# Optimization experiments

Hardware: AMD Instinct MI355X
Metric: run time of the kernel (lower is better)

Reference implementation:

```python
import jax, jax.numpy as jnp
import numpy as np

# SSD Detect post-processing constants (match init_kwargs)
NUM_CLASSES = 21
TOP_K = 200
CONF_THRESH = 0.95
NMS_THRESH = 0.45
M_CAND = 600      # candidate cap; chosen so all boxes passing CONF_THRESH fit (~437 expected)
NEG = -1e30


def setup_inputs() -> dict:
    key = jax.random.key(0)
    k1, k2, k3 = jax.random.split(key, 3)
    B, P, C = 8, 8732, NUM_CLASSES
    loc_data = jax.random.normal(k1, (B, P, 4), dtype=jnp.float32)
    conf_data = jax.random.uniform(k2, (B, P, C), dtype=jnp.float32)
    prior_data = jax.random.uniform(k3, (1, P, 4), dtype=jnp.float32)
    return {"loc_data": loc_data, "conf_data": conf_data, "prior_data": prior_data}


def _nms_lane(boxes_all, scores):
    """One (batch, class) lane. boxes_all: [P,4], scores: [P]. Returns [TOP_K, 5]."""
    pass_mask = scores > CONF_THRESH                       # [P]
    masked = jnp.where(pass_mask, scores, jnp.float32(NEG))
    vals, idx = jax.lax.top_k(masked, M_CAND)              # score-desc candidates (prior idx)
    valid = vals > jnp.float32(NEG / 2)                    # passed threshold
    cb = boxes_all[idx]                                    # [M,4] (x1,y1,x2,y2)
    x1, y1, x2, y2 = cb[:, 0], cb[:, 1], cb[:, 2], cb[:, 3]
    area = (x2 - x1) * (y2 - y1)                           # torchvision-style, no clamp
    xx1 = jnp.maximum(x1[:, None], x1[None, :])
    yy1 = jnp.maximum(y1[:, None], y1[None, :])
    xx2 = jnp.minimum(x2[:, None], x2[None, :])
    yy2 = jnp.minimum(y2[:, None], y2[None, :])
    inter = jnp.clip(xx2 - xx1, 0.0) * jnp.clip(yy2 - yy1, 0.0)
    iou = inter / (area[:, None] + area[None, :] - inter)  # [M,M]
    ar = jnp.arange(M_CAND)

    def body(i, supp):
        keep_i = valid[i] & jnp.logical_not(supp[i])
        return supp | (keep_i & (iou[i] > NMS_THRESH) & (ar > i))

    supp = jax.lax.fori_loop(0, M_CAND, body, jnp.zeros((M_CAND,), bool))
    keep = valid & jnp.logical_not(supp)
    order = jnp.argsort(jnp.logical_not(keep))             # stable: kept first, score order
    n = jnp.minimum(keep.sum(), TOP_K)                     # number of kept boxes (<= TOP_K)
    sel_prior = idx[order[:TOP_K]]                         # prior ids of kept (score order)
    slot_valid = jnp.arange(TOP_K) < n
    fp = jnp.argmax(pass_mask)                             # first prior passing threshold
    prior_ids = jnp.where(slot_valid, sel_prior, fp)       # pad with boxes[0] like torch
    out_scores = jnp.where(slot_valid, scores[prior_ids], 0.0)
    out = jnp.concatenate([out_scores[:, None], boxes_all[prior_ids]], axis=1)  # [K,5]
    return jnp.where(pass_mask.any(), out, jnp.zeros_like(out))


def _forward(loc_data, conf_data, prior_data):
    # prior_data is accepted per the torch signature but unused by the forward math.
    per_batch = jax.vmap(
        lambda boxes, conf_b: jax.vmap(lambda s: _nms_lane(boxes, s))(conf_b[:, 1:].T)
    )
    out_fg = per_batch(loc_data, conf_data)                # [B, C-1, K, 5]
    bg = jnp.zeros_like(out_fg[:, :1])                     # background class row stays 0
    return jnp.concatenate([bg, out_fg], axis=1)           # [B, C, K, 5]


def reference(loc_data, conf_data, prior_data):
    return _forward(loc_data, conf_data, prior_data)
```

## Files before the change

### kernel.cpp

```cpp
#include <hip/hip_runtime.h>
#include <float.h>
#include <math.h>


#define P_PRIORS  8732
#define C_CLASSES 21
#define B_BATCH   8
#define TOPK      200
#define MCAND     600
#define CONF_T    0.95f
#define NMS_T     0.45f
#define NB        64
#define MINB      0x3F733334u

__device__ __forceinline__ uint64_t pack_key(float sc, int p) {
    return ((uint64_t)__float_as_uint(sc) << 32) | (uint32_t)(~(uint32_t)p);
}
__device__ __forceinline__ int bucket_of(uint64_t key) {
    unsigned d = (unsigned)(key >> 32) - MINB;
    int b = (int)(d >> 14);
    return b < (NB - 1) ? b : (NB - 1);
}

#define IOU_ROW(BI, AI, MW, DIAG) do {                                   \
    float xx1 = fmaxf((BI).x, bj.x);                                     \
    float yy1 = fmaxf((BI).y, bj.y);                                     \
    float xx2 = fminf((BI).z, bj.z);                                     \
    float yy2 = fminf((BI).w, bj.w);                                     \
    float ww  = fmaxf(xx2 - xx1, 0.0f);                                  \
    float hh  = fmaxf(yy2 - yy1, 0.0f);                                  \
    float inter = ww * hh;                                               \
    float den   = ((AI) + aj) - inter;              \
    float iou   = inter / den;               \
    uint64_t m = __ballot(iou > NMS_T);                                  \
    if (k == c) m &= (DIAG);                                             \
    (MW) = (lid == k) ? m : (MW);                                        \
} while (0)

__device__ __forceinline__ void iou_chunk(
    int c, int wid, int lid, int M, int kmax,
    const float4* s_jb, const float* s_area, uint64_t* s_bm)
{
    const int i0 = (c << 6) + wid;
    const float4 b0 = s_jb[i0],      b1 = s_jb[i0 + 16],
                 b2 = s_jb[i0 + 32], b3 = s_jb[i0 + 48];
    const float  a0 = s_area[i0],      a1 = s_area[i0 + 16],
                 a2 = s_area[i0 + 32], a3 = s_area[i0 + 48];
    const uint64_t d0 = ~0ull << (wid + 1);
    const uint64_t d1 = ~0ull << (wid + 17);
    const uint64_t d2 = ~0ull << (wid + 33);
    const uint64_t d3 = (wid == 15) ? 0ull : (~0ull << (wid + 49));
    uint64_t w0 = 0, w1 = 0, w2 = 0, w3 = 0;
    for (int k = c; k < kmax; ++k) {
        const float4 bj = s_jb[(k << 6) + lid];
        const float  aj = s_area[(k << 6) + lid];
        IOU_ROW(b0, a0, w0, d0);
        IOU_ROW(b1, a1, w1, d1);
        IOU_ROW(b2, a2, w2, d2);
        IOU_ROW(b3, a3, w3, d3);
    }
    if (lid >= c && lid < kmax) {
        if (i0      < M) s_bm[(size_t)(i0     ) * 10 + lid] = w0;
        if (i0 + 16 < M) s_bm[(size_t)(i0 + 16) * 10 + lid] = w1;
        if (i0 + 32 < M) s_bm[(size_t)(i0 + 32) * 10 + lid] = w2;
        if (i0 + 48 < M) s_bm[(size_t)(i0 + 48) * 10 + lid] = w3;
    }
}

__global__ __launch_bounds__(1024) void detect_one(
    const float* __restrict__ loc, const float* __restrict__ conf,
    float* __restrict__ out)
{
    const int b   = blockIdx.x & 7;
    const int cls = blockIdx.x >> 3;
    const int tid = threadIdx.x;
    float* o = out + ((size_t)(b * C_CLASSES + cls)) * TOPK * 5;

    if (cls == 0) {
        for (int k = tid; k < TOPK * 5; k += 1024) o[k] = 0.0f;
        return;
    }

    const float*  confb = conf + (size_t)b * P_PRIORS * C_CLASSES + cls;
    const float4* loc4  = (const float4*)(loc + (size_t)b * P_PRIORS * 4);

    __shared__ uint64_t s_bm[MCAND * 10];
    __shared__ float4   s_jb[640];
    __shared__ float    s_area[640];
    __shared__ float    s_ssc[MCAND];
    __shared__ int      s_bcnt[NB], s_bcur[NB], s_boff[NB];
    __shared__ int      s_cnt, s_fp;
    __shared__ uint64_t s_suppw[10], s_keepw[10];
    __shared__ int      s_prefix[10], s_n, s_mstop, s_done;

    uint64_t* s_k   = s_bm;
    uint64_t* s_g   = s_bm + 1024;
    uint64_t* s_srt = s_bm + 2048;

    if (tid < NB)                    s_bcnt[tid] = 0;
    else if (tid < 2 * NB)           s_bcur[tid - NB] = 0;
    else if (tid == 2 * NB)        { s_cnt = 0; s_fp = 0x7FFFFFFF; }
    __syncthreads();

    {
        const int lid = tid & 63;
        for (int p = tid; p < P_PRIORS; p += 1024) {
            float sc = confb[(size_t)p * C_CLASSES];
            bool pass = sc > CONF_T;
            uint64_t mask = __ballot(pass);
            if (mask != 0) {
                int leader = (int)__ffsll((unsigned long long)mask) - 1;
                int base = 0;
                if (lid == leader) {
                    base = atomicAdd(&s_cnt, __popcll(mask));
                    atomicMin(&s_fp, p);
                }
                base = __shfl(base, leader, 64);
                if (pass) {
                    int pos = base + __popcll(mask & ((1ull << lid) - 1ull));
                    if (pos < 1024) s_k[pos] = pack_key(sc, p);
                }
            }
        }
    }
    __syncthreads();
    int cnt = s_cnt; if (cnt > 1024) cnt = 1024;
    if (cnt == 0) {
        for (int k = tid; k < TOPK * 5; k += 1024) o[k] = 0.0f;
        return;
    }

    for (int t = tid; t < cnt; t += 1024)
        atomicAdd(&s_bcnt[bucket_of(s_k[t])], 1);
    __syncthreads();

    if (tid < 64) {
        int c = s_bcnt[63 - tid];
        int incl = c;
        #pragma unroll
        for (int d = 1; d < 64; d <<= 1) {
            int u = __shfl_up(incl, d, 64);
            if (tid >= d) incl += u;
        }
        s_boff[63 - tid] = incl - c;
    }
    __syncthreads();

    for (int t = tid; t < cnt; t += 1024) {
        uint64_t kt = s_k[t];
        int bb = bucket_of(kt);
        s_g[s_boff[bb] + atomicAdd(&s_bcur[bb], 1)] = kt;
    }
    __syncthreads();

    const int M = cnt < MCAND ? cnt : MCAND;
    {
        const int wid = tid >> 6, lid = tid & 63;
        for (int bb = wid; bb < NB; bb += 16) {
            int st = s_boff[bb], n = s_bcnt[bb];
            for (int e = lid; e < n; e += 64) {
                uint64_t kq = s_g[st + e];
                int r = st;
                for (int q = 0; q < n; ++q)
                    r += (s_g[st + q] > kq) ? 1 : 0;
                if (r < MCAND) s_srt[r] = kq;
            }
        }
    }
    __syncthreads();

    for (int i = tid; i < M; i += 1024) {
        uint64_t key = s_srt[i];
        int p = (int)(~(uint32_t)key);
        s_ssc[i]  = __uint_as_float((uint32_t)(key >> 32));
        float4 bx = loc4[p];
        s_jb[i]   = bx;
        s_area[i] = (bx.z - bx.x) * (bx.w - bx.y);
    }
    for (int i = M + tid; i < 640; i += 1024) {
        s_jb[i]   = make_float4(INFINITY, INFINITY, INFINITY, INFINITY);
        s_area[i] = INFINITY;
    }
    const int fp = s_fp;
    __syncthreads();

    const int kmax = (M + 63) >> 6;

    {
        const int wid = tid >> 6, lid = tid & 63;
        const int w   = (lid < 10) ? lid : 0;
        uint64_t supp = 0;
        int kept = 0, mstop = M;
        const int nch = kmax;

        iou_chunk(0, wid, lid, M, kmax, s_jb, s_area, s_bm);
        __syncthreads();

        for (int c = 0; c < nch; ++c) {
            if (wid == 0) {
                const int ibeg = c << 6;
                const int iend = min(ibeg + 64, M);
                uint64_t rb[8];
                #pragma unroll
                for (int d = 0; d < 8; ++d) {
                    int i = ibeg + d;
                    rb[d] = (i < iend) ? s_bm[(size_t)i * 10 + w] : 0;
                }
                for (int i = ibeg; i < iend; ++i) {
                    uint64_t row = rb[i & 7];
                    if (w < c) row = 0;
                    int ip = i + 8;
                    rb[i & 7] = (ip < iend) ? s_bm[(size_t)ip * 10 + w] : 0;
                    bool mybit = (w == c) && ((supp >> (i & 63)) & 1ull);
                    if (!__any((int)mybit)) {
                        supp |= row;
                        if (++kept == TOPK) { mstop = i + 1; break; }
                    }
                }
                if (lid == 0) s_done = (kept >= TOPK) ? 1 : 0;
                if (kept < TOPK && c + 1 < nch)
                    iou_chunk(c + 1, 0, lid, M, kmax, s_jb, s_area, s_bm);
            } else if (c + 1 < nch) {
                iou_chunk(c + 1, wid, lid, M, kmax, s_jb, s_area, s_bm);
            }
            __syncthreads();
            if (s_done) break;
        }
        if (wid == 0) {
            if (lid < 10) s_suppw[lid] = supp;
            if (lid == 0) s_mstop = mstop;
        }
    }
    __syncthreads();

    if (tid == 0) {
        const int Me = s_mstop;
        int total = 0;
        for (int w = 0; w < 10; ++w) {
            uint64_t kw = 0;
            int rem = Me - (w << 6);
            if (rem > 0) {
                uint64_t vm = (rem >= 64) ? ~0ull : ((1ull << rem) - 1ull);
                kw = (~s_suppw[w]) & vm;
            }
            s_keepw[w]  = kw;
            s_prefix[w] = total;
            total += __popcll(kw);
        }
        s_n = total < TOPK ? total : TOPK;
    }
    __syncthreads();

    const int n  = s_n;
    const int Me = s_mstop;
    float4 fbox = loc4[fp];
    for (int k = tid; k < TOPK; k += 1024) {
        if (k >= n) {
            o[k * 5 + 0] = 0.0f;
            o[k * 5 + 1] = fbox.x; o[k * 5 + 2] = fbox.y;
            o[k * 5 + 3] = fbox.z; o[k * 5 + 4] = fbox.w;
        }
    }
    for (int t = tid; t < Me; t += 1024) {
        uint64_t kw = s_keepw[t >> 6];
        if ((kw >> (t & 63)) & 1ull) {
            int r = s_prefix[t >> 6] + __popcll(kw & ((1ull << (t & 63)) - 1ull));
            if (r < TOPK) {
                float4 bx = s_jb[t];
                o[r * 5 + 0] = s_ssc[t];
                o[r * 5 + 1] = bx.x; o[r * 5 + 2] = bx.y;
                o[r * 5 + 3] = bx.z; o[r * 5 + 4] = bx.w;
            }
        }
    }
}

extern "C" void kernel_launch(void* const* d_in, const int* in_sizes, int n_in,
                              void* d_out, int out_size, void* d_ws, size_t ws_size,
                              hipStream_t stream) {
    const float* loc  = (const float*)d_in[0];
    const float* conf = (const float*)d_in[1];
    float* out = (float*)d_out;
    (void)d_ws; (void)ws_size;

    detect_one<<<dim3(B_BATCH * C_CLASSES), dim3(1024), 0, stream>>>(loc, conf, out);
}
```

Measured before the change: 109.0 us.

## Replace wave vote in NMS scan with broadcast diagonal mask; batch conf loads

The serial NMS scan used to test the current row's suppression bit with a wave-wide __any vote on every candidate. It now keeps a wave-uniform copy of the diagonal suppression word, built from a new per-row diagonal mask array. This removes the cross-lane reduction from the critical serial loop. The change also preloads all 9 confidence values per thread before the ballots and folds the bucket histogram into the compaction pass, which drops one pass and one barrier. Finally, the division-based IoU test is replaced by a double-precision multiply compare, adding double arithmetic in exchange for avoiding the divide.

```diff
diff --git a/kernel.cpp b/kernel.cpp
--- a/kernel.cpp
+++ b/kernel.cpp
@@ -9,9 +9,9 @@
 #define TOPK      200
 #define MCAND     600
 #define CONF_T    0.95f
-#define NMS_T     0.45f
 #define NB        64
 #define MINB      0x3F733334u
+#define M_THR     ((double)0.45f + 0x1p-26)
 
 __device__ __forceinline__ uint64_t pack_key(float sc, int p) {
     return ((uint64_t)__float_as_uint(sc) << 32) | (uint32_t)(~(uint32_t)p);
@@ -22,42 +22,56 @@
     return b < (NB - 1) ? b : (NB - 1);
 }
 
-#define IOU_ROW(BI, AI, MW, DIAG) do {                                   \
-    float xx1 = fmaxf((BI).x, bj.x);                                     \
-    float yy1 = fmaxf((BI).y, bj.y);                                     \
-    float xx2 = fminf((BI).z, bj.z);                                     \
-    float yy2 = fminf((BI).w, bj.w);                                     \
-    float ww  = fmaxf(xx2 - xx1, 0.0f);                                  \
-    float hh  = fmaxf(yy2 - yy1, 0.0f);                                  \
-    float inter = ww * hh;                                               \
-    float den   = ((AI) + aj) - inter;              \
-    float iou   = inter / den;               \
-    uint64_t m = __ballot(iou > NMS_T);                                  \
-    if (k == c) m &= (DIAG);                                             \
-    (MW) = (lid == k) ? m : (MW);                                        \
-} while (0)
+__device__ __forceinline__ bool iou_gt(const float4 bi, float ai,
+                                       const float4 bj, float aj) {
+    float xx1 = fmaxf(bi.x, bj.x);
+    float yy1 = fmaxf(bi.y, bj.y);
+    float xx2 = fminf(bi.z, bj.z);
+    float yy2 = fminf(bi.w, bj.w);
+    float ww  = fmaxf(xx2 - xx1, 0.0f);
+    float hh  = fmaxf(yy2 - yy1, 0.0f);
+    float inter = ww * hh;
+    float den   = (ai + aj) - inter;
+    return ((int)__float_as_int(den) >= 0) &&
+           ((double)inter > M_THR * (double)den);
+}
 
 __device__ __forceinline__ void iou_chunk(
     int c, int wid, int lid, int M, int kmax,
-    const float4* s_jb, const float* s_area, uint64_t* s_bm)
+    const float4* s_jb, const float* s_area, uint64_t* s_bm, uint64_t* s_diag)
 {
     const int i0 = (c << 6) + wid;
     const float4 b0 = s_jb[i0],      b1 = s_jb[i0 + 16],
                  b2 = s_jb[i0 + 32], b3 = s_jb[i0 + 48];
     const float  a0 = s_area[i0],      a1 = s_area[i0 + 16],
                  a2 = s_area[i0 + 32], a3 = s_area[i0 + 48];
-    const uint64_t d0 = ~0ull << (wid + 1);
-    const uint64_t d1 = ~0ull << (wid + 17);
-    const uint64_t d2 = ~0ull << (wid + 33);
-    const uint64_t d3 = (wid == 15) ? 0ull : (~0ull << (wid + 49));
-    uint64_t w0 = 0, w1 = 0, w2 = 0, w3 = 0;
-    for (int k = c; k < kmax; ++k) {
+    uint64_t w0, w1, w2, w3;
+    {
+        const float4 bj = s_jb[(c << 6) + lid];
+        const float  aj = s_area[(c << 6) + lid];
+        uint64_t m0 = __ballot(iou_gt(b0, a0, bj, aj)) & (~0ull << (wid + 1));
+        uint64_t m1 = __ballot(iou_gt(b1, a1, bj, aj)) & (~0ull << (wid + 17));
+        uint64_t m2 = __ballot(iou_gt(b2, a2, bj, aj)) & (~0ull << (wid + 33));
+        uint64_t m3 = (wid == 15) ? 0ull
+                    : (__ballot(iou_gt(b3, a3, bj, aj)) & (~0ull << (wid + 49)));
+        w0 = (lid == c) ? m0 : 0;  w1 = (lid == c) ? m1 : 0;
+        w2 = (lid == c) ? m2 : 0;  w3 = (lid == c) ? m3 : 0;
+        if (lid == 0) {
+            s_diag[i0]      = m0;
+            s_diag[i0 + 16] = m1;
+            s_diag[i0 + 32] = m2;
+            s_diag[i0 + 48] = m3;
+        }
+    }
+    for (int k = c + 1; k < kmax; ++k) {
         const float4 bj = s_jb[(k << 6) + lid];
         const float  aj = s_area[(k << 6) + lid];
-        IOU_ROW(b0, a0, w0, d0);
-        IOU_ROW(b1, a1, w1, d1);
-        IOU_ROW(b2, a2, w2, d2);
-        IOU_ROW(b3, a3, w3, d3);
+        uint64_t m0 = __ballot(iou_gt(b0, a0, bj, aj));
+        uint64_t m1 = __ballot(iou_gt(b1, a1, bj, aj));
+        uint64_t m2 = __ballot(iou_gt(b2, a2, bj, aj));
+        uint64_t m3 = __ballot(iou_gt(b3, a3, bj, aj));
+        w0 = (lid == k) ? m0 : w0;  w1 = (lid == k) ? m1 : w1;
+        w2 = (lid == k) ? m2 : w2;  w3 = (lid == k) ? m3 : w3;
     }
     if (lid >= c && lid < kmax) {
         if (i0      < M) s_bm[(size_t)(i0     ) * 10 + lid] = w0;
@@ -85,6 +99,7 @@
     const float4* loc4  = (const float4*)(loc + (size_t)b * P_PRIORS * 4);
 
     __shared__ uint64_t s_bm[MCAND * 10];
+    __shared__ uint64_t s_diag[640];
     __shared__ float4   s_jb[640];
     __shared__ float    s_area[640];
     __shared__ float    s_ssc[MCAND];
@@ -104,9 +119,18 @@
 
     {
         const int lid = tid & 63;
-        for (int p = tid; p < P_PRIORS; p += 1024) {
-            float sc = confb[(size_t)p * C_CLASSES];
-            bool pass = sc > CONF_T;
+        float v[9];
+        #pragma unroll
+        for (int r = 0; r < 8; ++r)
+            v[r] = confb[(size_t)(tid + (r << 10)) * C_CLASSES];
+        {
+            int p8 = tid + 8192;
+            v[8] = (p8 < P_PRIORS) ? confb[(size_t)p8 * C_CLASSES] : 0.0f;
+        }
+        #pragma unroll
+        for (int r = 0; r < 9; ++r) {
+            int p = tid + (r << 10);
+            bool pass = v[r] > CONF_T;
             uint64_t mask = __ballot(pass);
             if (mask != 0) {
                 int leader = (int)__ffsll((unsigned long long)mask) - 1;
@@ -118,7 +142,11 @@
                 base = __shfl(base, leader, 64);
                 if (pass) {
                     int pos = base + __popcll(mask & ((1ull << lid) - 1ull));
-                    if (pos < 1024) s_k[pos] = pack_key(sc, p);
+                    if (pos < 1024) {
+                        uint64_t key = pack_key(v[r], p);
+                        s_k[pos] = key;
+                        atomicAdd(&s_bcnt[bucket_of(key)], 1);
+                    }
                 }
             }
         }
@@ -129,10 +157,6 @@
         for (int k = tid; k < TOPK * 5; k += 1024) o[k] = 0.0f;
         return;
     }
-
-    for (int t = tid; t < cnt; t += 1024)
-        atomicAdd(&s_bcnt[bucket_of(s_k[t])], 1);
-    __syncthreads();
 
     if (tid < 64) {
         int c = s_bcnt[63 - tid];
@@ -161,6 +185,7 @@
             for (int e = lid; e < n; e += 64) {
                 uint64_t kq = s_g[st + e];
                 int r = st;
+                #pragma unroll 4
                 for (int q = 0; q < n; ++q)
                     r += (s_g[st + q] > kq) ? 1 : 0;
                 if (r < MCAND) s_srt[r] = kq;
@@ -193,35 +218,45 @@
         int kept = 0, mstop = M;
         const int nch = kmax;
 
-        iou_chunk(0, wid, lid, M, kmax, s_jb, s_area, s_bm);
+        iou_chunk(0, wid, lid, M, kmax, s_jb, s_area, s_bm, s_diag);
         __syncthreads();
 
         for (int c = 0; c < nch; ++c) {
             if (wid == 0) {
                 const int ibeg = c << 6;
                 const int iend = min(ibeg + 64, M);
-                uint64_t rb[8];
+                uint64_t cur;
+                {
+                    int lo = __shfl((int)(uint32_t)supp, c, 64);
+                    int hi = __shfl((int)(uint32_t)(supp >> 32), c, 64);
+                    cur = ((uint64_t)(uint32_t)hi << 32) | (uint32_t)lo;
+                }
+                uint64_t rb[8], db[8];
                 #pragma unroll
                 for (int d = 0; d < 8; ++d) {
                     int i = ibeg + d;
                     rb[d] = (i < iend) ? s_bm[(size_t)i * 10 + w] : 0;
+                    db[d] = (i < iend) ? s_diag[i] : 0;
                 }
                 for (int i = ibeg; i < iend; ++i) {
-                    uint64_t row = rb[i & 7];
+                    uint64_t row  = rb[i & 7];
+                    uint64_t rowc = db[i & 7];
                     if (w < c) row = 0;
                     int ip = i + 8;
                     rb[i & 7] = (ip < iend) ? s_bm[(size_t)ip * 10 + w] : 0;
-                    bool mybit = (w == c) && ((supp >> (i & 63)) & 1ull);
-                    if (!__any((int)mybit)) {
+                    db[i & 7] = (ip < iend) ? s_diag[ip] : 0;
+                    bool keep = !((cur >> (i & 63)) & 1ull);
+                    if (keep) {
+                        cur  |= rowc;
                         supp |= row;
                         if (++kept == TOPK) { mstop = i + 1; break; }
                     }
                 }
                 if (lid == 0) s_done = (kept >= TOPK) ? 1 : 0;
                 if (kept < TOPK && c + 1 < nch)
-                    iou_chunk(c + 1, 0, lid, M, kmax, s_jb, s_area, s_bm);
+                    iou_chunk(c + 1, 0, lid, M, kmax, s_jb, s_area, s_bm, s_diag);
             } else if (c + 1 < nch) {
-                iou_chunk(c + 1, wid, lid, M, kmax, s_jb, s_area, s_bm);
+                iou_chunk(c + 1, wid, lid, M, kmax, s_jb, s_area, s_bm, s_diag);
             }
             __syncthreads();
             if (s_done) break;
```

Result: slower. 125.6 us (+15.3%).
